# Kernel optimization log

Hardware: AMD Instinct MI355X
Metric: run time of the kernel (lower is better)

Reference implementation:

```python
import jax, jax.numpy as jnp
import numpy as np

N = 50000      # nodes
E = 800000     # edges (before self loops)
F_IN = 64
H = 128
OUT = 1
G = 512        # graphs in batch
NEG_SLOPE = 0.2


def setup_inputs() -> dict:
    key = jax.random.key(0)
    ks = jax.random.split(key, 16)
    s_in = 1.0 / np.sqrt(F_IN)
    s_h = 1.0 / np.sqrt(H)
    return {
        "x": jax.random.normal(ks[0], (N, F_IN), jnp.float32),
        "edge_index": jax.random.randint(ks[1], (2, E), 0, N, jnp.int64),
        "edge_weight": jax.random.uniform(ks[2], (E,), jnp.float32),
        "batch": jnp.sort(jax.random.randint(ks[3], (N,), 0, G, jnp.int64)),
        # GATv2 layer 1 (lin_l, lin_r, att, bias)
        "Wl1": jax.random.normal(ks[4], (F_IN, H), jnp.float32) * s_in,
        "bl1": jnp.zeros((H,), jnp.float32),
        "Wr1": jax.random.normal(ks[5], (F_IN, H), jnp.float32) * s_in,
        "br1": jnp.zeros((H,), jnp.float32),
        "att1": jax.random.normal(ks[6], (H,), jnp.float32) * s_h,
        "b1": jnp.zeros((H,), jnp.float32),
        # GATv2 layer 2
        "Wl2": jax.random.normal(ks[7], (H, H), jnp.float32) * s_h,
        "bl2": jnp.zeros((H,), jnp.float32),
        "Wr2": jax.random.normal(ks[8], (H, H), jnp.float32) * s_h,
        "br2": jnp.zeros((H,), jnp.float32),
        "att2": jax.random.normal(ks[9], (H,), jnp.float32) * s_h,
        "b2": jnp.zeros((H,), jnp.float32),
        # final linear head
        "Wlin": jax.random.normal(ks[10], (H, OUT), jnp.float32) * s_h,
        "blin": jnp.zeros((OUT,), jnp.float32),
    }


def gatv2_conv(x, src, dst, Wl, bl, Wr, br, att, bias):
    """PyG GATv2Conv, heads=1: alpha = softmax_dst(att . leaky_relu(xl[src]+xr[dst]));
    out[dst] = sum alpha * xl[src] + bias. Self loops already in (src, dst)."""
    xl = x @ Wl + bl                       # [N,H]  source transform
    xr = x @ Wr + br                       # [N,H]  destination transform
    e = xl[src] + xr[dst]                  # [Etot,H]
    logits = jax.nn.leaky_relu(e, NEG_SLOPE) @ att   # [Etot]
    # segment softmax over destination nodes (self loops -> every node nonempty)
    m = jax.ops.segment_max(logits, dst, num_segments=N)
    ea = jnp.exp(logits - m[dst])
    denom = jax.ops.segment_sum(ea, dst, num_segments=N)
    alpha = ea / denom[dst]
    out = jax.ops.segment_sum(alpha[:, None] * xl[src], dst, num_segments=N)
    return out + bias


def reference(x, edge_index, edge_weight, batch,
              Wl1, bl1, Wr1, br1, att1, b1,
              Wl2, bl2, Wr2, br2, att2, b2,
              Wlin, blin):
    # add self loops (GATv2Conv default add_self_loops=True); edge_weight unused by GATv2
    loops = jnp.arange(N, dtype=edge_index.dtype)
    src = jnp.concatenate([edge_index[0], loops])
    dst = jnp.concatenate([edge_index[1], loops])

    h = jax.nn.relu(gatv2_conv(x, src, dst, Wl1, bl1, Wr1, br1, att1, b1))
    h = jax.nn.relu(gatv2_conv(h, src, dst, Wl2, bl2, Wr2, br2, att2, b2))

    # global mean pool over graphs
    sums = jax.ops.segment_sum(h, batch, num_segments=G)          # [G,H]
    cnt = jax.ops.segment_sum(jnp.ones((N,), h.dtype), batch, num_segments=G)
    pooled = sums / jnp.maximum(cnt, 1.0)[:, None]

    return pooled @ Wlin + blin                                   # [G,OUT]
```

## Files before the change

kernel.cpp:

```cpp
#include <hip/hip_runtime.h>
#include <hip/hip_fp16.h>
#include <math.h>

#define N_NODES 50000
#define N_EDGES 800000
#define F_IN    64
#define H_DIM   128
#define N_GRAPH 512
#define NEG_SLOPE 0.2f

typedef __attribute__((ext_vector_type(8))) short short8;
typedef __attribute__((ext_vector_type(4))) float f32x4;
typedef __attribute__((ext_vector_type(2))) float f32x2;
typedef _Float16 h2 __attribute__((ext_vector_type(2)));
typedef _Float16 h8 __attribute__((ext_vector_type(8)));

#define NBIN   196
#define NBLK1  391
#define NBB    (NBIN * NBLK1)
#define SCANA_NB ((NBB + 255) / 256)

__device__ __forceinline__ void bsplit(float v, unsigned short& h, unsigned short& l) {
    unsigned u = __float_as_uint(v);
    h = (unsigned short)(u >> 16);
    float hf = __uint_as_float(u & 0xFFFF0000u);
    float r = v - hf;
    l = (unsigned short)(__float_as_uint(r) >> 16);
}

#define NB_PW 192
__global__ __launch_bounds__(256) void k_prep(
    const float* __restrict__ Wl1, const float* __restrict__ Wr1,
    const float* __restrict__ Wl2, const float* __restrict__ Wr2,
    const int* __restrict__ dst,
    unsigned short* __restrict__ WThi, unsigned short* __restrict__ WTlo,
    unsigned short* __restrict__ WT2f,
    int* __restrict__ lrank, int* __restrict__ bcnt)
{
    __shared__ int cnt_lds[NBIN];
    const int bid = blockIdx.x, tid = threadIdx.x;
    if (bid < NB_PW) {
        int idx = bid * 256 + tid;
        if (idx < 49152) {
            const float* W; int K, li, base, o;
            if (idx < 8192)       { W = Wl1; K = 64;  li = idx;         base = 0;     o = 0; }
            else if (idx < 16384) { W = Wr1; K = 64;  li = idx - 8192;  base = 0;     o = 1; }
            else if (idx < 32768) { W = Wl2; K = 128; li = idx - 16384; base = 16384; o = 0; }
            else                  { W = Wr2; K = 128; li = idx - 32768; base = 16384; o = 1; }
            int c = li / K, k = li - c * K;
            int g = c >> 4, n16 = c & 15;
            int kkblk = k >> 5, quad = (k >> 3) & 3, j = k & 7;
            int off = base + kkblk * 8192 + o * 4096 + g * 512 + (quad * 16 + n16) * 8 + j;
            float wv = W[k * 128 + c];
            if (base == 0) {
                unsigned short h, l;
                bsplit(wv, h, l);
                WThi[off] = h; WTlo[off] = l;
            } else {
                __half hv = __float2half(wv);
                WT2f[off - 16384] = *(unsigned short*)&hv;
            }
        }
    } else {
        const int b2 = bid - NB_PW;
        if (tid < NBIN) cnt_lds[tid] = 0;
        __syncthreads();
#pragma unroll
        for (int it = 0; it < 8; ++it) {
            int e = b2 * 2048 + it * 256 + tid;
            if (e < N_EDGES) {
                int d = dst[e];
                lrank[e] = atomicAdd(&cnt_lds[d >> 8], 1);
            }
        }
        __syncthreads();
        if (tid < NBIN) bcnt[tid * NBLK1 + b2] = cnt_lds[tid];
    }
}

__global__ __launch_bounds__(256) void k_scanA(const int* __restrict__ bcnt,
                                               int* __restrict__ bbase,
                                               int* __restrict__ partials) {
    __shared__ int s[256];
    int t = threadIdx.x, gid = blockIdx.x * 256 + t;
    int v = (gid < NBB) ? bcnt[gid] : 0;
    s[t] = v;
    __syncthreads();
    for (int off = 1; off < 256; off <<= 1) {
        int x = (t >= off) ? s[t - off] : 0;
        __syncthreads();
        s[t] += x;
        __syncthreads();
    }
    if (gid < NBB) bbase[gid] = s[t] - v;
    if (t == 255) partials[blockIdx.x] = s[t];
}

__global__ __launch_bounds__(256) void k_scanB(int* __restrict__ bbase,
                                               const int* __restrict__ partials) {
    __shared__ int red[256];
    const int t = threadIdx.x, b = blockIdx.x;
    int acc = 0;
    for (int j = t; j < b; j += 256) acc += partials[j];
    red[t] = acc;
    __syncthreads();
    for (int off = 128; off > 0; off >>= 1) {
        if (t < off) red[t] += red[t + off];
        __syncthreads();
    }
    int base = red[0];
    int gid = b * 256 + t;
    if (gid < NBB) bbase[gid] += base;
}

__global__ __launch_bounds__(256) void k_bin2(const int* __restrict__ src,
                                              const int* __restrict__ dst,
                                              const int* __restrict__ lrank,
                                              const int* __restrict__ bbase,
                                              unsigned* __restrict__ ebin) {
    int e = blockIdx.x * 256 + threadIdx.x;
    if (e < N_EDGES) {
        int d = dst[e];
        int pos = bbase[(d >> 8) * NBLK1 + (e >> 11)] + lrank[e];
        ebin[pos] = (unsigned)src[e] | ((unsigned)(d & 255) << 16);
    }
}

__global__ __launch_bounds__(256) void k_bin3(const unsigned* __restrict__ ebin,
                                              const int* __restrict__ bbase,
                                              int* __restrict__ offsets,
                                              int* __restrict__ col_src) {
    __shared__ int cnt2[256];
    __shared__ int sc[256];
    __shared__ int cur[256];
    const int b = blockIdx.x, t = threadIdx.x;
    const int lo = bbase[b * NBLK1];
    const int hi = (b == NBIN - 1) ? N_EDGES : bbase[(b + 1) * NBLK1];

    cnt2[t] = 0;
    __syncthreads();
    for (int pos = lo + t; pos < hi; pos += 256) {
        unsigned u = ebin[pos];
        atomicAdd(&cnt2[u >> 16], 1);
    }
    __syncthreads();
    int v = cnt2[t];
    sc[t] = v;
    __syncthreads();
    for (int off = 1; off < 256; off <<= 1) {
        int x = (t >= off) ? sc[t - off] : 0;
        __syncthreads();
        sc[t] += x;
        __syncthreads();
    }
    int myoff = lo + sc[t] - v;
    int node = b * 256 + t;
    if (node < N_NODES) offsets[node] = myoff;
    cur[t] = myoff;
    if (b == NBIN - 1 && t == 0) offsets[N_NODES] = N_EDGES;
    __syncthreads();
    for (int pos = lo + t; pos < hi; pos += 256) {
        unsigned u = ebin[pos];
        int p = atomicAdd(&cur[u >> 16], 1);
        col_src[p] = (int)(u & 0xFFFFu);
    }
}

#define APITCH 40
#define GB_GEMM ((N_NODES + 63) / 64)

__global__ __launch_bounds__(256, 4) void k_gemm_f32(
    const float* __restrict__ Xf,
    const unsigned short* __restrict__ WThi, const unsigned short* __restrict__ WTlo,
    const float* __restrict__ bl, const float* __restrict__ br,
    unsigned short* __restrict__ OL, unsigned short* __restrict__ OR_, int K)
{
    __shared__ __align__(16) unsigned short Ah[64 * APITCH];
    __shared__ __align__(16) unsigned short Al[64 * APITCH];

    const int tid  = threadIdx.x;
    const int wv   = tid >> 6;
    const int lane = tid & 63;
    const int n16  = lane & 15;
    const int quad = lane >> 4;
    const int row0 = blockIdx.x * 64;

    f32x4 acc[4][2][2];
#pragma unroll
    for (int r = 0; r < 4; ++r)
#pragma unroll
        for (int c = 0; c < 2; ++c)
#pragma unroll
            for (int o = 0; o < 2; ++o) acc[r][c][o] = (f32x4)0.f;

    for (int kk = 0; kk < K; kk += 32) {
        {
            int r = tid >> 2, sub = tid & 3;
            int grow = row0 + r;
            float4 v0 = make_float4(0.f, 0.f, 0.f, 0.f);
            float4 v1 = make_float4(0.f, 0.f, 0.f, 0.f);
            if (grow < N_NODES) {
                const float* s = Xf + (size_t)grow * K + kk + sub * 8;
                v0 = *(const float4*)s;
                v1 = *(const float4*)(s + 4);
            }
            union { unsigned short s[8]; uint4 u; } Hh, Ll;
            bsplit(v0.x, Hh.s[0], Ll.s[0]); bsplit(v0.y, Hh.s[1], Ll.s[1]);
            bsplit(v0.z, Hh.s[2], Ll.s[2]); bsplit(v0.w, Hh.s[3], Ll.s[3]);
            bsplit(v1.x, Hh.s[4], Ll.s[4]); bsplit(v1.y, Hh.s[5], Ll.s[5]);
            bsplit(v1.z, Hh.s[6], Ll.s[6]); bsplit(v1.w, Hh.s[7], Ll.s[7]);
            *(uint4*)(Ah + r * APITCH + sub * 8) = Hh.u;
            *(uint4*)(Al + r * APITCH + sub * 8) = Ll.u;
        }
        __syncthreads();

        const unsigned short* wb_h = WThi + (size_t)(kk >> 5) * 8192;
        const unsigned short* wb_l = WTlo + (size_t)(kk >> 5) * 8192;
        short8 bh[2][2], bo[2][2];
#pragma unroll
        for (int c = 0; c < 2; ++c)
#pragma unroll
            for (int o = 0; o < 2; ++o) {
                size_t off = (size_t)o * 4096 + (size_t)(wv * 2 + c) * 512 + (size_t)lane * 8;
                bh[c][o] = *(const short8*)(wb_h + off);
                bo[c][o] = *(const short8*)(wb_l + off);
            }
#pragma unroll
        for (int r = 0; r < 4; ++r) {
            int rl = r * 16 + n16;
            short8 ah = *(const short8*)(Ah + rl * APITCH + quad * 8);
            short8 al = *(const short8*)(Al + rl * APITCH + quad * 8);
#pragma unroll
            for (int c = 0; c < 2; ++c)
#pragma unroll
                for (int o = 0; o < 2; ++o) {
                    f32x4 t = acc[r][c][o];
                    t = __builtin_amdgcn_mfma_f32_16x16x32_bf16(ah, bh[c][o], t, 0, 0, 0);
                    t = __builtin_amdgcn_mfma_f32_16x16x32_bf16(ah, bo[c][o], t, 0, 0, 0);
                    t = __builtin_amdgcn_mfma_f32_16x16x32_bf16(al, bh[c][o], t, 0, 0, 0);
                    acc[r][c][o] = t;
                }
        }
        __syncthreads();
    }

#pragma unroll
    for (int r = 0; r < 4; ++r)
#pragma unroll
        for (int c = 0; c < 2; ++c)
#pragma unroll
            for (int o = 0; o < 2; ++o) {
                int col = wv * 32 + c * 16 + n16;
                float bb = (o ? br : bl)[col];
                unsigned short* O = o ? OR_ : OL;
#pragma unroll
                for (int g = 0; g < 4; ++g) {
                    int grow = row0 + r * 16 + quad * 4 + g;
                    if (grow < N_NODES) {
                        __half hv = __float2half(acc[r][c][o][g] + bb);
                        O[(size_t)grow * 128 + col] = *(unsigned short*)&hv;
                    }
                }
            }
}

__global__ __launch_bounds__(256, 4) void k_gemm_f16(
    const unsigned short* __restrict__ X,
    const unsigned short* __restrict__ WT2f,
    const float* __restrict__ bl, const float* __restrict__ br,
    unsigned short* __restrict__ OL, unsigned short* __restrict__ OR_)
{
    __shared__ __align__(16) unsigned short Ah[64 * APITCH];

    const int tid  = threadIdx.x;
    const int wv   = tid >> 6;
    const int lane = tid & 63;
    const int n16  = lane & 15;
    const int quad = lane >> 4;
    const int row0 = blockIdx.x * 64;

    f32x4 acc[4][2][2];
#pragma unroll
    for (int r = 0; r < 4; ++r)
#pragma unroll
        for (int c = 0; c < 2; ++c)
#pragma unroll
            for (int o = 0; o < 2; ++o) acc[r][c][o] = (f32x4)0.f;

    for (int kk = 0; kk < 128; kk += 32) {
        {
            int r = tid >> 2, sub = tid & 3;
            int grow = row0 + r;
            uint4 v = make_uint4(0u, 0u, 0u, 0u);
            if (grow < N_NODES)
                v = *(const uint4*)(X + (size_t)grow * 128 + kk + sub * 8);
            *(uint4*)(Ah + r * APITCH + sub * 8) = v;
        }
        __syncthreads();

        const unsigned short* wb = WT2f + (size_t)(kk >> 5) * 8192;
        h8 bf[2][2];
#pragma unroll
        for (int c = 0; c < 2; ++c)
#pragma unroll
            for (int o = 0; o < 2; ++o) {
                size_t off = (size_t)o * 4096 + (size_t)(wv * 2 + c) * 512 + (size_t)lane * 8;
                bf[c][o] = *(const h8*)(wb + off);
            }
#pragma unroll
        for (int r = 0; r < 4; ++r) {
            int rl = r * 16 + n16;
            h8 ah = *(const h8*)(Ah + rl * APITCH + quad * 8);
#pragma unroll
            for (int c = 0; c < 2; ++c)
#pragma unroll
                for (int o = 0; o < 2; ++o)
                    acc[r][c][o] = __builtin_amdgcn_mfma_f32_16x16x32_f16(
                        ah, bf[c][o], acc[r][c][o], 0, 0, 0);
        }
        __syncthreads();
    }

#pragma unroll
    for (int r = 0; r < 4; ++r)
#pragma unroll
        for (int c = 0; c < 2; ++c)
#pragma unroll
            for (int o = 0; o < 2; ++o) {
                int col = wv * 32 + c * 16 + n16;
                float bb = (o ? br : bl)[col];
                unsigned short* O = o ? OR_ : OL;
#pragma unroll
                for (int g = 0; g < 4; ++g) {
                    int grow = row0 + r * 16 + quad * 4 + g;
                    if (grow < N_NODES) {
                        __half hv = __float2half(acc[r][c][o][g] + bb);
                        O[(size_t)grow * 128 + col] = *(unsigned short*)&hv;
                    }
                }
            }
}

__device__ __forceinline__ float red16dpp(float v) {
    v += __int_as_float(__builtin_amdgcn_update_dpp(
             0, __float_as_int(v), 0xB1, 0xF, 0xF, true));
    v += __int_as_float(__builtin_amdgcn_update_dpp(
             0, __float_as_int(v), 0x4E, 0xF, 0xF, true));
    v += __int_as_float(__builtin_amdgcn_update_dpp(
             0, __float_as_int(v), 0x141, 0xF, 0xF, true));
    v += __int_as_float(__builtin_amdgcn_update_dpp(
             0, __float_as_int(v), 0x140, 0xF, 0xF, true));
    return v;
}

__device__ __forceinline__ float dot8lk_h(uint4 u, const h2 r[4], const h2 a[4]) {
    const h2 ns = { (_Float16)NEG_SLOPE, (_Float16)NEG_SLOPE };
    float s = 0.f;
    h2 x0 = __builtin_bit_cast(h2, u.x);
    h2 x1 = __builtin_bit_cast(h2, u.y);
    h2 x2 = __builtin_bit_cast(h2, u.z);
    h2 x3 = __builtin_bit_cast(h2, u.w);
    h2 e0 = x0 + r[0];
    h2 e1 = x1 + r[1];
    h2 e2 = x2 + r[2];
    h2 e3 = x3 + r[3];
    h2 l0 = __builtin_elementwise_max(e0, e0 * ns);
    h2 l1 = __builtin_elementwise_max(e1, e1 * ns);
    h2 l2 = __builtin_elementwise_max(e2, e2 * ns);
    h2 l3 = __builtin_elementwise_max(e3, e3 * ns);
    s = __builtin_amdgcn_fdot2(l0, a[0], s, false);
    s = __builtin_amdgcn_fdot2(l1, a[1], s, false);
    s = __builtin_amdgcn_fdot2(l2, a[2], s, false);
    s = __builtin_amdgcn_fdot2(l3, a[3], s, false);
    return s;
}

__global__ __launch_bounds__(256) void k_edge(
    const unsigned short* __restrict__ xl, const unsigned short* __restrict__ xr,
    const float* __restrict__ att, const float* __restrict__ bias,
    const int* __restrict__ offsets, const int* __restrict__ col_src,
    unsigned short* __restrict__ outH)
{
    int d = blockIdx.x * 4 + (threadIdx.x >> 6);
    if (d >= N_NODES) return;
    const int lane = threadIdx.x & 63;
    const int q = lane >> 4;
    const int t = lane & 15;
    const size_t dim0 = (size_t)t * 8;

    h2 rr[4], aa[4];
    {
        uint4 ur = *(const uint4*)(xr + (size_t)d * 128 + dim0);
        rr[0] = __builtin_bit_cast(h2, ur.x);
        rr[1] = __builtin_bit_cast(h2, ur.y);
        rr[2] = __builtin_bit_cast(h2, ur.z);
        rr[3] = __builtin_bit_cast(h2, ur.w);
        const float4 a0 = *(const float4*)(att + dim0);
        const float4 a1 = *(const float4*)(att + dim0 + 4);
        h2 w0 = { (_Float16)a0.x, (_Float16)a0.y }; aa[0] = w0;
        h2 w1 = { (_Float16)a0.z, (_Float16)a0.w }; aa[1] = w1;
        h2 w2 = { (_Float16)a1.x, (_Float16)a1.y }; aa[2] = w2;
        h2 w3 = { (_Float16)a1.z, (_Float16)a1.w }; aa[3] = w3;
    }

    uint4 uxs = *(const uint4*)(xl + (size_t)d * 128 + dim0);
    float sl = red16dpp(dot8lk_h(uxs, rr, aa));

    float m = sl, thr = sl + 8.f;
    float lsum = (q == 0) ? 1.f : 0.f;
    f32x2 acc[4];
    {
        float2 sa = __half22float2(*(__half2*)&uxs.x);
        float2 sb = __half22float2(*(__half2*)&uxs.y);
        float2 sc_ = __half22float2(*(__half2*)&uxs.z);
        float2 sd = __half22float2(*(__half2*)&uxs.w);
        f32x2 z = {0.f, 0.f};
        f32x2 v0 = {sa.x, sa.y}; acc[0] = (q == 0) ? v0 : z;
        f32x2 v1 = {sb.x, sb.y}; acc[1] = (q == 0) ? v1 : z;
        f32x2 v2 = {sc_.x, sc_.y}; acc[2] = (q == 0) ? v2 : z;
        f32x2 v3 = {sd.x, sd.y}; acc[3] = (q == 0) ? v3 : z;
    }

    const int ibeg = offsets[d], iend = offsets[d + 1];
    int ia = ibeg + q;
    bool vA = ia < iend;
    int sA = vA ? col_src[ia] : d;
    uint4 uA = *(const uint4*)(xl + (size_t)sA * 128 + dim0);
    int ib = ia + 4;
    bool vB = ib < iend;
    int sB = vB ? col_src[ib] : d;

    for (int base = ibeg; base < iend; base += 4) {
        uint4 uB = *(const uint4*)(xl + (size_t)sB * 128 + dim0);
        int ic = base + 8 + q;
        bool vC = ic < iend;
        int sC = vC ? col_src[ic] : d;

        float logit = red16dpp(dot8lk_h(uA, rr, aa));
        if (__builtin_expect(logit > thr, 0)) {
            float sc = __expf(m - logit);
            lsum *= sc;
#pragma unroll
            for (int j = 0; j < 4; ++j) acc[j] = acc[j] * sc;
            m = logit; thr = logit + 8.f;
        }
        float w = vA ? __expf(logit - m) : 0.f;
        lsum += w;
        {
            __half2* hp = (__half2*)&uA;
#pragma unroll
            for (int j = 0; j < 4; ++j) {
                float2 xf = __half22float2(hp[j]);
                acc[j].x = fmaf(xf.x, w, acc[j].x);
                acc[j].y = fmaf(xf.y, w, acc[j].y);
            }
        }

        uA = uB; vA = vB; sB = sC; vB = vC;
    }

    float M = m;
    M = fmaxf(M, __shfl_xor(M, 16));
    M = fmaxf(M, __shfl_xor(M, 32));
    float sc = __expf(m - M);
    lsum *= sc;
    f32x2 sc2 = {sc, sc};
#pragma unroll
    for (int j = 0; j < 4; ++j) acc[j] = acc[j] * sc2;
#pragma unroll
    for (int off = 16; off <= 32; off <<= 1) {
        lsum += __shfl_xor(lsum, off);
#pragma unroll
        for (int j = 0; j < 4; ++j) {
            acc[j].x += __shfl_xor(acc[j].x, off);
            acc[j].y += __shfl_xor(acc[j].y, off);
        }
    }

    if (q == 0) {
        float inv = 1.f / lsum;
        const float4 b0 = *(const float4*)(bias + dim0);
        const float4 b1 = *(const float4*)(bias + dim0 + 4);
        float bv[8] = {b0.x, b0.y, b0.z, b0.w, b1.x, b1.y, b1.z, b1.w};
        union { __half2 h[4]; uint4 u; } O;
#pragma unroll
        for (int j = 0; j < 4; ++j) {
            float v0 = fmaxf(fmaf(acc[j].x, inv, bv[2 * j]), 0.f);
            float v1 = fmaxf(fmaf(acc[j].y, inv, bv[2 * j + 1]), 0.f);
            O.h[j] = __floats2half2_rn(v0, v1);
        }
        *(uint4*)(outH + (size_t)d * 128 + dim0) = O.u;
    }
}

__global__ __launch_bounds__(256) void k_pool(
    const unsigned short* __restrict__ H,
    const int* __restrict__ batch,
    float* __restrict__ psum, float* __restrict__ pcnt)
{
    const int tid = threadIdx.x;
    const int tx = tid & 31;
    const int ty = tid >> 5;
    const int n0 = blockIdx.x * 64;
    const int d0 = tx * 4;

    float4 acc = make_float4(0.f, 0.f, 0.f, 0.f);
    int cur = -1, crun = 0;
#pragma unroll
    for (int it = 0; it < 8; ++it) {
        int n = n0 + it * 8 + ty;
        if (n < N_NODES) {
            int g = batch[n];
            if (g != cur) {
                if (cur >= 0) {
                    atomicAdd(&psum[cur * 128 + d0 + 0], acc.x);
                    atomicAdd(&psum[cur * 128 + d0 + 1], acc.y);
                    atomicAdd(&psum[cur * 128 + d0 + 2], acc.z);
                    atomicAdd(&psum[cur * 128 + d0 + 3], acc.w);
                    if (tx == 0) atomicAdd(&pcnt[cur], (float)crun);
                }
                cur = g; acc = make_float4(0.f, 0.f, 0.f, 0.f); crun = 0;
            }
            uint2 hv = *(const uint2*)(H + (size_t)n * 128 + d0);
            float2 a = __half22float2(*(__half2*)&hv.x);
            float2 b = __half22float2(*(__half2*)&hv.y);
            acc.x += a.x; acc.y += a.y; acc.z += b.x; acc.w += b.y;
            crun++;
        }
    }
    if (cur >= 0) {
        atomicAdd(&psum[cur * 128 + d0 + 0], acc.x);
        atomicAdd(&psum[cur * 128 + d0 + 1], acc.y);
        atomicAdd(&psum[cur * 128 + d0 + 2], acc.z);
        atomicAdd(&psum[cur * 128 + d0 + 3], acc.w);
        if (tx == 0) atomicAdd(&pcnt[cur], (float)crun);
    }
}

__global__ __launch_bounds__(256) void k_head(
    const float* __restrict__ psum, const float* __restrict__ pcnt,
    const float* __restrict__ Wlin, const float* __restrict__ blin,
    float* __restrict__ out)
{
    int g = blockIdx.x * 4 + (threadIdx.x >> 6);
    if (g >= N_GRAPH) return;
    int lane = threadIdx.x & 63;
    float c = fmaxf(pcnt[g], 1.f);
    float2 s = *(const float2*)(psum + (size_t)g * 128 + lane * 2);
    float p = (s.x * Wlin[lane * 2] + s.y * Wlin[lane * 2 + 1]) / c;
#pragma unroll
    for (int off = 32; off > 0; off >>= 1) p += __shfl_xor(p, off);
    if (lane == 0) out[g] = p + blin[0];
}

extern "C" void kernel_launch(void* const* d_in, const int* in_sizes, int n_in,
                              void* d_out, int out_size, void* d_ws, size_t ws_size,
                              hipStream_t stream) {
    const float* x     = (const float*)d_in[0];
    const int*   ei    = (const int*)d_in[1];
    const int*   batch = (const int*)d_in[3];
    const float* Wl1 = (const float*)d_in[4],  *bl1 = (const float*)d_in[5];
    const float* Wr1 = (const float*)d_in[6],  *br1 = (const float*)d_in[7];
    const float* att1= (const float*)d_in[8],  *b1  = (const float*)d_in[9];
    const float* Wl2 = (const float*)d_in[10], *bl2 = (const float*)d_in[11];
    const float* Wr2 = (const float*)d_in[12], *br2 = (const float*)d_in[13];
    const float* att2= (const float*)d_in[14], *b2  = (const float*)d_in[15];
    const float* Wlin= (const float*)d_in[16], *blin= (const float*)d_in[17];
    float* out = (float*)d_out;

    const int* src = ei;
    const int* dst = ei + N_EDGES;

    char* p = (char*)d_ws;
    auto carve = [&](size_t bytes) {
        void* r = (void*)p;
        p += (bytes + 255) & ~(size_t)255;
        return r;
    };
    unsigned short* bufA   = (unsigned short*)carve((size_t)N_NODES * 128 * 2);
    unsigned short* bufB   = (unsigned short*)carve((size_t)N_NODES * 128 * 2);
    unsigned short* H      = (unsigned short*)carve((size_t)N_NODES * 128 * 2);
    unsigned short* WThi   = (unsigned short*)carve(16384 * 2);
    unsigned short* WTlo   = (unsigned short*)carve(16384 * 2);
    unsigned short* WT2f   = (unsigned short*)carve(32768 * 2);
    int*            offsets= (int*)carve((size_t)(N_NODES + 1) * 4);
    int*            lrank  = (int*)carve((size_t)N_EDGES * 4);
    int*            bcnt   = (int*)carve((size_t)NBB * 4);
    int*            bbase  = (int*)carve((size_t)NBB * 4);
    int*            partials=(int*)carve(SCANA_NB * 4);
    unsigned*       ebin   = (unsigned*)carve((size_t)N_EDGES * 4);
    int*            col_src= (int*)carve((size_t)N_EDGES * 4);
    char* zb = (char*)carve(262144 + 2048);
    float* psum   = (float*)zb;
    float* pcnt   = (float*)(zb + 262144);
    const size_t zbytes = 262144 + 2048;

    hipMemsetAsync(zb, 0, zbytes, stream);

    k_prep<<<NB_PW + NBLK1, 256, 0, stream>>>(
        Wl1, Wr1, Wl2, Wr2, dst, WThi, WTlo, WT2f, lrank, bcnt);

    k_gemm_f32<<<GB_GEMM, 256, 0, stream>>>(x, WThi, WTlo,
                                            bl1, br1, bufA, bufB, F_IN);

    k_scanA<<<SCANA_NB, 256, 0, stream>>>(bcnt, bbase, partials);
    k_scanB<<<SCANA_NB, 256, 0, stream>>>(bbase, partials);
    k_bin2 <<<(N_EDGES + 255) / 256, 256, 0, stream>>>(src, dst, lrank, bbase, ebin);
    k_bin3 <<<NBIN, 256, 0, stream>>>(ebin, bbase, offsets, col_src);

    k_edge<<<(N_NODES + 3) / 4, 256, 0, stream>>>(
        bufA, bufB, att1, b1, offsets, col_src, H);
    k_gemm_f16<<<GB_GEMM, 256, 0, stream>>>(H, WT2f, bl2, br2, bufA, bufB);
    k_edge<<<(N_NODES + 3) / 4, 256, 0, stream>>>(
        bufA, bufB, att2, b2, offsets, col_src, H);
    k_pool<<<(N_NODES + 63) / 64, 256, 0, stream>>>(H, batch, psum, pcnt);
    k_head<<<(N_GRAPH + 3) / 4, 256, 0, stream>>>(psum, pcnt, Wlin, blin, out);
}
```

Measured before the change: 258.2 us.

## Use single fp16 MFMA for layer-1 GEMM and fold partial scan into binning

Layer 1 used to emulate fp32 with three split-bf16 MFMAs per tile. It now converts x and the weights to fp16 and runs one MFMA per tile, sharing a templated kernel with layer 2. Separately, the k_scanB launch is removed: k_bin2 and k_bin3 each rescan the block partials in LDS and add the chunk base themselves. This cuts MFMA work and one launch, but gives up the near-fp32 accuracy of the first projection and repeats a small scan in every bin2 block.

```diff
diff --git a/kernel.cpp b/kernel.cpp
--- a/kernel.cpp
+++ b/kernel.cpp
@@ -9,7 +9,6 @@
 #define N_GRAPH 512
 #define NEG_SLOPE 0.2f
 
-typedef __attribute__((ext_vector_type(8))) short short8;
 typedef __attribute__((ext_vector_type(4))) float f32x4;
 typedef __attribute__((ext_vector_type(2))) float f32x2;
 typedef _Float16 h2 __attribute__((ext_vector_type(2)));
@@ -19,22 +18,13 @@
 #define NBLK1  391
 #define NBB    (NBIN * NBLK1)
 #define SCANA_NB ((NBB + 255) / 256)
-
-__device__ __forceinline__ void bsplit(float v, unsigned short& h, unsigned short& l) {
-    unsigned u = __float_as_uint(v);
-    h = (unsigned short)(u >> 16);
-    float hf = __uint_as_float(u & 0xFFFF0000u);
-    float r = v - hf;
-    l = (unsigned short)(__float_as_uint(r) >> 16);
-}
 
 #define NB_PW 192
 __global__ __launch_bounds__(256) void k_prep(
     const float* __restrict__ Wl1, const float* __restrict__ Wr1,
     const float* __restrict__ Wl2, const float* __restrict__ Wr2,
     const int* __restrict__ dst,
-    unsigned short* __restrict__ WThi, unsigned short* __restrict__ WTlo,
-    unsigned short* __restrict__ WT2f,
+    unsigned short* __restrict__ WTf,
     int* __restrict__ lrank, int* __restrict__ bcnt)
 {
     __shared__ int cnt_lds[NBIN];
@@ -51,15 +41,8 @@
             int g = c >> 4, n16 = c & 15;
             int kkblk = k >> 5, quad = (k >> 3) & 3, j = k & 7;
             int off = base + kkblk * 8192 + o * 4096 + g * 512 + (quad * 16 + n16) * 8 + j;
-            float wv = W[k * 128 + c];
-            if (base == 0) {
-                unsigned short h, l;
-                bsplit(wv, h, l);
-                WThi[off] = h; WTlo[off] = l;
-            } else {
-                __half hv = __float2half(wv);
-                WT2f[off - 16384] = *(unsigned short*)&hv;
-            }
+            __half hv = __float2half(W[k * 128 + c]);
+            WTf[off] = *(unsigned short*)&hv;
         }
     } else {
         const int b2 = bid - NB_PW;
@@ -96,46 +79,64 @@
     if (t == 255) partials[blockIdx.x] = s[t];
 }
 
-__global__ __launch_bounds__(256) void k_scanB(int* __restrict__ bbase,
-                                               const int* __restrict__ partials) {
-    __shared__ int red[256];
-    const int t = threadIdx.x, b = blockIdx.x;
-    int acc = 0;
-    for (int j = t; j < b; j += 256) acc += partials[j];
-    red[t] = acc;
-    __syncthreads();
-    for (int off = 128; off > 0; off >>= 1) {
-        if (t < off) red[t] += red[t + off];
-        __syncthreads();
-    }
-    int base = red[0];
-    int gid = b * 256 + t;
-    if (gid < NBB) bbase[gid] += base;
+__device__ __forceinline__ void scan_partials(const int* __restrict__ partials,
+                                              int* __restrict__ sp, int t) {
+    sp[t]       = (t < SCANA_NB) ? partials[t] : 0;
+    sp[t + 256] = (t + 256 < SCANA_NB) ? partials[t + 256] : 0;
+    __syncthreads();
+    for (int off = 1; off < 512; off <<= 1) {
+        int a = (t >= off) ? sp[t - off] : 0;
+        int b = sp[t + 256 - off];
+        __syncthreads();
+        sp[t] += a;
+        sp[t + 256] += b;
+        __syncthreads();
+    }
 }
 
 __global__ __launch_bounds__(256) void k_bin2(const int* __restrict__ src,
                                               const int* __restrict__ dst,
                                               const int* __restrict__ lrank,
                                               const int* __restrict__ bbase,
+                                              const int* __restrict__ partials,
                                               unsigned* __restrict__ ebin) {
-    int e = blockIdx.x * 256 + threadIdx.x;
+    __shared__ int sp[512];
+    const int t = threadIdx.x;
+    scan_partials(partials, sp, t);
+    int e = blockIdx.x * 256 + t;
     if (e < N_EDGES) {
         int d = dst[e];
-        int pos = bbase[(d >> 8) * NBLK1 + (e >> 11)] + lrank[e];
+        int idx = (d >> 8) * NBLK1 + (e >> 11);
+        int chunk = idx >> 8;
+        int cbase = chunk ? sp[chunk - 1] : 0;
+        int pos = bbase[idx] + cbase + lrank[e];
         ebin[pos] = (unsigned)src[e] | ((unsigned)(d & 255) << 16);
     }
 }
 
 __global__ __launch_bounds__(256) void k_bin3(const unsigned* __restrict__ ebin,
                                               const int* __restrict__ bbase,
+                                              const int* __restrict__ partials,
                                               int* __restrict__ offsets,
                                               int* __restrict__ col_src) {
+    __shared__ int sp[512];
     __shared__ int cnt2[256];
     __shared__ int sc[256];
     __shared__ int cur[256];
     const int b = blockIdx.x, t = threadIdx.x;
-    const int lo = bbase[b * NBLK1];
-    const int hi = (b == NBIN - 1) ? N_EDGES : bbase[(b + 1) * NBLK1];
+
+    scan_partials(partials, sp, t);
+    int lo, hi;
+    {
+        int idx0 = b * NBLK1, c0 = idx0 >> 8;
+        lo = bbase[idx0] + (c0 ? sp[c0 - 1] : 0);
+        if (b == NBIN - 1) hi = N_EDGES;
+        else {
+            int idx1 = (b + 1) * NBLK1, c1 = idx1 >> 8;
+            hi = bbase[idx1] + (c1 ? sp[c1 - 1] : 0);
+        }
+    }
+    __syncthreads();
 
     cnt2[t] = 0;
     __syncthreads();
@@ -169,14 +170,15 @@
 #define APITCH 40
 #define GB_GEMM ((N_NODES + 63) / 64)
 
-__global__ __launch_bounds__(256, 4) void k_gemm_f32(
+template <bool F32SRC>
+__global__ __launch_bounds__(256, 4) void k_gemm16(
     const float* __restrict__ Xf,
-    const unsigned short* __restrict__ WThi, const unsigned short* __restrict__ WTlo,
+    const unsigned short* __restrict__ Xh,
+    const unsigned short* __restrict__ WTf,
     const float* __restrict__ bl, const float* __restrict__ br,
     unsigned short* __restrict__ OL, unsigned short* __restrict__ OR_, int K)
 {
     __shared__ __align__(16) unsigned short Ah[64 * APITCH];
-    __shared__ __align__(16) unsigned short Al[64 * APITCH];
 
     const int tid  = threadIdx.x;
     const int wv   = tid >> 6;
@@ -197,108 +199,30 @@
         {
             int r = tid >> 2, sub = tid & 3;
             int grow = row0 + r;
-            float4 v0 = make_float4(0.f, 0.f, 0.f, 0.f);
-            float4 v1 = make_float4(0.f, 0.f, 0.f, 0.f);
-            if (grow < N_NODES) {
-                const float* s = Xf + (size_t)grow * K + kk + sub * 8;
-                v0 = *(const float4*)s;
-                v1 = *(const float4*)(s + 4);
+            if (F32SRC) {
+                float4 v0 = make_float4(0.f, 0.f, 0.f, 0.f);
+                float4 v1 = make_float4(0.f, 0.f, 0.f, 0.f);
+                if (grow < N_NODES) {
+                    const float* s = Xf + (size_t)grow * K + kk + sub * 8;
+                    v0 = *(const float4*)s;
+                    v1 = *(const float4*)(s + 4);
+                }
+                union { __half2 h[4]; uint4 u; } cv;
+                cv.h[0] = __floats2half2_rn(v0.x, v0.y);
+                cv.h[1] = __floats2half2_rn(v0.z, v0.w);
+                cv.h[2] = __floats2half2_rn(v1.x, v1.y);
+                cv.h[3] = __floats2half2_rn(v1.z, v1.w);
+                *(uint4*)(Ah + r * APITCH + sub * 8) = cv.u;
+            } else {
+                uint4 v = make_uint4(0u, 0u, 0u, 0u);
+                if (grow < N_NODES)
+                    v = *(const uint4*)(Xh + (size_t)grow * K + kk + sub * 8);
+                *(uint4*)(Ah + r * APITCH + sub * 8) = v;
             }
-            union { unsigned short s[8]; uint4 u; } Hh, Ll;
-            bsplit(v0.x, Hh.s[0], Ll.s[0]); bsplit(v0.y, Hh.s[1], Ll.s[1]);
-            bsplit(v0.z, Hh.s[2], Ll.s[2]); bsplit(v0.w, Hh.s[3], Ll.s[3]);
-            bsplit(v1.x, Hh.s[4], Ll.s[4]); bsplit(v1.y, Hh.s[5], Ll.s[5]);
-            bsplit(v1.z, Hh.s[6], Ll.s[6]); bsplit(v1.w, Hh.s[7], Ll.s[7]);
-            *(uint4*)(Ah + r * APITCH + sub * 8) = Hh.u;
-            *(uint4*)(Al + r * APITCH + sub * 8) = Ll.u;
-        }
-        __syncthreads();
-
-        const unsigned short* wb_h = WThi + (size_t)(kk >> 5) * 8192;
-        const unsigned short* wb_l = WTlo + (size_t)(kk >> 5) * 8192;
-        short8 bh[2][2], bo[2][2];
-#pragma unroll
-        for (int c = 0; c < 2; ++c)
-#pragma unroll
-            for (int o = 0; o < 2; ++o) {
-                size_t off = (size_t)o * 4096 + (size_t)(wv * 2 + c) * 512 + (size_t)lane * 8;
-                bh[c][o] = *(const short8*)(wb_h + off);
-                bo[c][o] = *(const short8*)(wb_l + off);
-            }
-#pragma unroll
-        for (int r = 0; r < 4; ++r) {
-            int rl = r * 16 + n16;
-            short8 ah = *(const short8*)(Ah + rl * APITCH + quad * 8);
-            short8 al = *(const short8*)(Al + rl * APITCH + quad * 8);
-#pragma unroll
-            for (int c = 0; c < 2; ++c)
-#pragma unroll
-                for (int o = 0; o < 2; ++o) {
-                    f32x4 t = acc[r][c][o];
-                    t = __builtin_amdgcn_mfma_f32_16x16x32_bf16(ah, bh[c][o], t, 0, 0, 0);
-                    t = __builtin_amdgcn_mfma_f32_16x16x32_bf16(ah, bo[c][o], t, 0, 0, 0);
-                    t = __builtin_amdgcn_mfma_f32_16x16x32_bf16(al, bh[c][o], t, 0, 0, 0);
-                    acc[r][c][o] = t;
-                }
-        }
-        __syncthreads();
-    }
-
-#pragma unroll
-    for (int r = 0; r < 4; ++r)
-#pragma unroll
-        for (int c = 0; c < 2; ++c)
-#pragma unroll
-            for (int o = 0; o < 2; ++o) {
-                int col = wv * 32 + c * 16 + n16;
-                float bb = (o ? br : bl)[col];
-                unsigned short* O = o ? OR_ : OL;
-#pragma unroll
-                for (int g = 0; g < 4; ++g) {
-                    int grow = row0 + r * 16 + quad * 4 + g;
-                    if (grow < N_NODES) {
-                        __half hv = __float2half(acc[r][c][o][g] + bb);
-                        O[(size_t)grow * 128 + col] = *(unsigned short*)&hv;
-                    }
-                }
-            }
-}
-
-__global__ __launch_bounds__(256, 4) void k_gemm_f16(
-    const unsigned short* __restrict__ X,
-    const unsigned short* __restrict__ WT2f,
-    const float* __restrict__ bl, const float* __restrict__ br,
-    unsigned short* __restrict__ OL, unsigned short* __restrict__ OR_)
-{
-    __shared__ __align__(16) unsigned short Ah[64 * APITCH];
-
-    const int tid  = threadIdx.x;
-    const int wv   = tid >> 6;
-    const int lane = tid & 63;
-    const int n16  = lane & 15;
-    const int quad = lane >> 4;
-    const int row0 = blockIdx.x * 64;
-
-    f32x4 acc[4][2][2];
-#pragma unroll
-    for (int r = 0; r < 4; ++r)
-#pragma unroll
-        for (int c = 0; c < 2; ++c)
-#pragma unroll
-            for (int o = 0; o < 2; ++o) acc[r][c][o] = (f32x4)0.f;
-
-    for (int kk = 0; kk < 128; kk += 32) {
-        {
-            int r = tid >> 2, sub = tid & 3;
-            int grow = row0 + r;
-            uint4 v = make_uint4(0u, 0u, 0u, 0u);
-            if (grow < N_NODES)
-                v = *(const uint4*)(X + (size_t)grow * 128 + kk + sub * 8);
-            *(uint4*)(Ah + r * APITCH + sub * 8) = v;
-        }
-        __syncthreads();
-
-        const unsigned short* wb = WT2f + (size_t)(kk >> 5) * 8192;
+        }
+        __syncthreads();
+
+        const unsigned short* wb = WTf + (size_t)(kk >> 5) * 8192;
         h8 bf[2][2];
 #pragma unroll
         for (int c = 0; c < 2; ++c)
@@ -580,9 +504,7 @@
     unsigned short* bufA   = (unsigned short*)carve((size_t)N_NODES * 128 * 2);
     unsigned short* bufB   = (unsigned short*)carve((size_t)N_NODES * 128 * 2);
     unsigned short* H      = (unsigned short*)carve((size_t)N_NODES * 128 * 2);
-    unsigned short* WThi   = (unsigned short*)carve(16384 * 2);
-    unsigned short* WTlo   = (unsigned short*)carve(16384 * 2);
-    unsigned short* WT2f   = (unsigned short*)carve(32768 * 2);
+    unsigned short* WTf    = (unsigned short*)carve(49152 * 2);
     int*            offsets= (int*)carve((size_t)(N_NODES + 1) * 4);
     int*            lrank  = (int*)carve((size_t)N_EDGES * 4);
     int*            bcnt   = (int*)carve((size_t)NBB * 4);
@@ -598,19 +520,20 @@
     hipMemsetAsync(zb, 0, zbytes, stream);
 
     k_prep<<<NB_PW + NBLK1, 256, 0, stream>>>(
-        Wl1, Wr1, Wl2, Wr2, dst, WThi, WTlo, WT2f, lrank, bcnt);
-
-    k_gemm_f32<<<GB_GEMM, 256, 0, stream>>>(x, WThi, WTlo,
-                                            bl1, br1, bufA, bufB, F_IN);
+        Wl1, Wr1, Wl2, Wr2, dst, WTf, lrank, bcnt);
+
+    k_gemm16<true><<<GB_GEMM, 256, 0, stream>>>(
+        x, nullptr, WTf, bl1, br1, bufA, bufB, F_IN);
 
     k_scanA<<<SCANA_NB, 256, 0, stream>>>(bcnt, bbase, partials);
-    k_scanB<<<SCANA_NB, 256, 0, stream>>>(bbase, partials);
-    k_bin2 <<<(N_EDGES + 255) / 256, 256, 0, stream>>>(src, dst, lrank, bbase, ebin);
-    k_bin3 <<<NBIN, 256, 0, stream>>>(ebin, bbase, offsets, col_src);
+    k_bin2 <<<(N_EDGES + 255) / 256, 256, 0, stream>>>(
+        src, dst, lrank, bbase, partials, ebin);
+    k_bin3 <<<NBIN, 256, 0, stream>>>(ebin, bbase, partials, offsets, col_src);
 
     k_edge<<<(N_NODES + 3) / 4, 256, 0, stream>>>(
         bufA, bufB, att1, b1, offsets, col_src, H);
-    k_gemm_f16<<<GB_GEMM, 256, 0, stream>>>(H, WT2f, bl2, br2, bufA, bufB);
+    k_gemm16<false><<<GB_GEMM, 256, 0, stream>>>(
+        nullptr, H, WTf + 16384, bl2, br2, bufA, bufB, H_DIM);
     k_edge<<<(N_NODES + 3) / 4, 256, 0, stream>>>(
         bufA, bufB, att2, b2, offsets, col_src, H);
     k_pool<<<(N_NODES + 63) / 64, 256, 0, stream>>>(H, batch, psum, pcnt);
```

Result: no change. 260.6 us, median of 2 (+0.9%).
